# Kernel optimization log

Measured on AMD Instinct MI355X. Metric: run time of the kernel, lower is better.

## Reference

```python
import jax, jax.numpy as jnp
import numpy as np

N_BATCH = 128   # C: number of PWL channels / generator batch
N_PTS = 32768   # N: samples per channel
K_PWL = 20      # breakpoints per piecewise-linear function
LATENT = 8
HID = 8
EPS = 1e-7


def _mlp(z, W1, b1, W2, b2):
    # torch mlp: Linear -> Tanh -> Linear -> Tanh
    h = jnp.tanh(z @ W1 + b1)
    return jnp.tanh(h @ W2 + b2)


def _normalize01(a):
    # per-row min/max normalization, a: [C, N]
    a = a - a.min(axis=1, keepdims=True)
    return a / a.max(axis=1, keepdims=True)


def _calibrate1d(x, xp, yp):
    # x: [N, C], xp/yp: [C, K]
    N, C = x.shape
    K = xp.shape[1]
    bp = jnp.concatenate([x[:, :, None], jnp.broadcast_to(xp[None], (N, C, K))], axis=2)  # [N,C,K+1]
    order = jnp.argsort(bp, axis=2)                       # [N,C,K+1]
    sorted_bp = jnp.take_along_axis(bp, order, axis=2)
    x_idx = jnp.argmin(order, axis=2)                     # rank of x among breakpoints
    cand = x_idx - 1
    start_idx = jnp.where(x_idx == 0, 1, jnp.where(x_idx == K, K - 2, cand))
    end_idx = jnp.where(start_idx == cand, start_idx + 2, start_idx + 1)
    start_x = jnp.take_along_axis(sorted_bp, start_idx[..., None], axis=2)[..., 0]
    end_x = jnp.take_along_axis(sorted_bp, end_idx[..., None], axis=2)[..., 0]
    start_idx2 = jnp.where(x_idx == 0, 0, jnp.where(x_idx == K, K - 2, cand))
    yp_e = jnp.broadcast_to(yp[None], (N, C, K))
    start_y = jnp.take_along_axis(yp_e, start_idx2[..., None], axis=2)[..., 0]
    end_y = jnp.take_along_axis(yp_e, (start_idx2 + 1)[..., None], axis=2)[..., 0]
    return start_y + (x - start_x) * (end_y - start_y) / (end_x - start_x + EPS)


def setup_inputs() -> dict:
    key = jax.random.key(0)
    ks = jax.random.split(key, 16)
    s = 0.5
    f32 = jnp.float32
    return {
        "zf": jax.random.normal(ks[0], (N_BATCH, LATENT), f32),
        "zx": jax.random.normal(ks[1], (N_BATCH, N_PTS, LATENT), f32),
        "ze": jax.random.normal(ks[2], (N_BATCH, N_PTS, LATENT), f32),
        "Wx1": jax.random.normal(ks[3], (LATENT, HID), f32) * s,
        "bx1": jax.random.normal(ks[4], (HID,), f32) * s,
        "Wx2": jax.random.normal(ks[5], (HID, 1), f32) * s,
        "bx2": jax.random.normal(ks[6], (1,), f32) * s,
        "We1": jax.random.normal(ks[7], (LATENT, HID), f32) * s,
        "be1": jax.random.normal(ks[8], (HID,), f32) * s,
        "We2": jax.random.normal(ks[9], (HID, 1), f32) * s,
        "be2": jax.random.normal(ks[10], (1,), f32) * s,
        "Wf1": jax.random.normal(ks[11], (LATENT, HID), f32) * s,
        "bf1": jax.random.normal(ks[12], (HID,), f32) * s,
        "Wf2": jax.random.normal(ks[13], (HID, K_PWL), f32) * s,
        "bf2": jax.random.normal(ks[14], (K_PWL,), f32) * s,
        "directions": jax.random.randint(ks[15], (N_BATCH,), 0, 2) > 0,
    }


def reference(zf, zx, ze, Wx1, bx1, Wx2, bx2, We1, be1, We2, be2, Wf1, bf1, Wf2, bf2, directions):
    # gen_f: random ascending/descending monotone PWL per channel
    pts = _mlp(zf, Wf1, bf1, Wf2, bf2)                        # [C, K]
    asc = jnp.sort(pts, axis=1)
    yp = jnp.where(directions[:, None], asc, asc[:, ::-1])    # [C, K]
    xp = jnp.broadcast_to(jnp.linspace(0.0, 1.0, K_PWL, dtype=pts.dtype)[None, :], yp.shape)
    # forward_x: cause variable, per-channel normalized to [0,1]
    x = _mlp(zx, Wx1, bx1, Wx2, bx2)[..., 0]                  # [C, N]
    x = _normalize01(x).T                                     # [N, C]
    # forward_e: standardized noise (global mean / unbiased std)
    e = _mlp(ze, We1, be1, We2, be2)[..., 0].T                # [N, C]
    e = (e - e.mean()) / e.std(ddof=1)
    # forward_y
    y = _calibrate1d(x, xp, yp) + 0.1 * e                     # [N, C]
    return y
```

## Files before the change

### kernel.cpp

```cpp
#include <hip/hip_runtime.h>

#define C_CH  128
#define NP    32768
#define K_PWL 20
#define LAT   8
#define HID   8
#define SLOTS 32
#define P1PTS 2

__device__ __forceinline__ float fast_tanh(float x) {
    float e = __expf(2.0f * x);
    return fmaf(-2.0f, __builtin_amdgcn_rcpf(e + 1.0f), 1.0f);
}

__device__ __forceinline__ unsigned fenc(float f) {
    unsigned u = __float_as_uint(f);
    return (u & 0x80000000u) ? ~u : (u | 0x80000000u);
}
__device__ __forceinline__ float fdec(unsigned e) {
    unsigned u = (e & 0x80000000u) ? (e ^ 0x80000000u) : ~e;
    return __uint_as_float(u);
}

__device__ __forceinline__ float mlp_eval(const float* W, float4 r0, float4 r1) {
    float acc = W[80];
    #pragma unroll
    for (int j = 0; j < HID; j++) {
        float hh = W[64 + j];
        hh = fmaf(r0.x, W[0 * 8 + j], hh);
        hh = fmaf(r0.y, W[1 * 8 + j], hh);
        hh = fmaf(r0.z, W[2 * 8 + j], hh);
        hh = fmaf(r0.w, W[3 * 8 + j], hh);
        hh = fmaf(r1.x, W[4 * 8 + j], hh);
        hh = fmaf(r1.y, W[5 * 8 + j], hh);
        hh = fmaf(r1.z, W[6 * 8 + j], hh);
        hh = fmaf(r1.w, W[7 * 8 + j], hh);
        acc = fmaf(fast_tanh(hh), W[72 + j], acc);
    }
    return fast_tanh(acc);
}

__global__ void prep(const float* __restrict__ zf,
                     const float* __restrict__ Wf1, const float* __restrict__ bf1,
                     const float* __restrict__ Wf2, const float* __restrict__ bf2,
                     const unsigned char* __restrict__ dirs_raw,
                     float* __restrict__ ypw,
                     unsigned* cminE, unsigned* cmaxE, double* sums) {
    int t = threadIdx.x;
    if (t < C_CH) { cminE[t] = 0xFFFFFFFFu; cmaxE[t] = 0u; }
    if (t < 2 * SLOTS) sums[t] = 0.0;

    __shared__ int is_i32;
    if (t == 0) {
        const int* di = (const int*)dirs_raw;
        int ok = 1;
        for (int i = 0; i < 32; i++) { int v = di[i]; if (v != 0 && v != 1) ok = 0; }
        is_i32 = ok;
    }
    __syncthreads();
    if (t >= C_CH) return;
    int c = t;

    float z[LAT];
    #pragma unroll
    for (int l = 0; l < LAT; l++) z[l] = zf[c * LAT + l];
    float h[HID];
    #pragma unroll
    for (int j = 0; j < HID; j++) {
        float a = bf1[j];
        #pragma unroll
        for (int l = 0; l < LAT; l++) a = fmaf(z[l], Wf1[l * HID + j], a);
        h[j] = fast_tanh(a);
    }
    float p[K_PWL];
    #pragma unroll
    for (int k = 0; k < K_PWL; k++) {
        float a = bf2[k];
        #pragma unroll
        for (int j = 0; j < HID; j++) a = fmaf(h[j], Wf2[j * K_PWL + k], a);
        p[k] = fast_tanh(a);
    }
    for (int i = 1; i < K_PWL; i++) {
        float key = p[i];
        int j = i - 1;
        while (j >= 0 && p[j] > key) { p[j + 1] = p[j]; j--; }
        p[j + 1] = key;
    }
    int dir = is_i32 ? (((const int*)dirs_raw)[c] != 0) : (dirs_raw[c] != 0);
    for (int k = 0; k < K_PWL; k++)
        ypw[c * K_PWL + k] = dir ? p[k] : p[K_PWL - 1 - k];
}

__global__ __launch_bounds__(256, 8)
void pass1t(const float* __restrict__ zx, const float* __restrict__ ze,
            const float* __restrict__ Wx1, const float* __restrict__ bx1,
            const float* __restrict__ Wx2, const float* __restrict__ bx2,
            const float* __restrict__ We1, const float* __restrict__ be1,
            const float* __restrict__ We2, const float* __restrict__ be2,
            float* __restrict__ xtile, float* __restrict__ etile,
            unsigned* __restrict__ cminE, unsigned* __restrict__ cmaxE,
            double* __restrict__ sums) {
    __shared__ float sw[162];
    int t = threadIdx.x;
    if (t < 64)       sw[t] = Wx1[t];
    else if (t < 72)  sw[t] = bx1[t - 64];
    else if (t < 80)  sw[t] = Wx2[t - 72];
    else if (t == 80) sw[80] = bx2[0];
    else if (t < 145) sw[t] = We1[t - 81];
    else if (t < 153) sw[t] = be1[t - 145];
    else if (t < 161) sw[t] = We2[t - 153];
    else if (t == 161) sw[161] = be2[0];
    __syncthreads();

    int c = blockIdx.y;
    int n0 = blockIdx.x * (256 * P1PTS) + t;
    size_t row = (size_t)c * NP;
    const float4* zx4 = (const float4*)(zx + row * LAT);
    const float4* ze4 = (const float4*)(ze + row * LAT);

    float4 ax[P1PTS][2], ae[P1PTS][2];
    #pragma unroll
    for (int k = 0; k < P1PTS; k++) {
        int n = n0 + k * 256;
        ax[k][0] = zx4[2 * n];  ax[k][1] = zx4[2 * n + 1];
        ae[k][0] = ze4[2 * n];  ae[k][1] = ze4[2 * n + 1];
    }

    float xv[P1PTS], ev[P1PTS];
    #pragma unroll
    for (int k = 0; k < P1PTS; k++) xv[k] = mlp_eval(sw, ax[k][0], ax[k][1]);
    #pragma unroll
    for (int k = 0; k < P1PTS; k++) ev[k] = mlp_eval(sw + 81, ae[k][0], ae[k][1]);

    float mn = xv[0], mx = xv[0], s = 0.f, s2 = 0.f;
    int cbase = c * 32;
    #pragma unroll
    for (int k = 0; k < P1PTS; k++) {
        int n = n0 + k * 256;
        int addr = (n >> 5) * (C_CH * 32) + cbase + (n & 31);
        xtile[addr] = xv[k];
        etile[addr] = ev[k];
        mn = fminf(mn, xv[k]); mx = fmaxf(mx, xv[k]);
        s += ev[k]; s2 += ev[k] * ev[k];
    }

    #pragma unroll
    for (int o = 32; o > 0; o >>= 1) {
        mn = fminf(mn, __shfl_down(mn, o));
        mx = fmaxf(mx, __shfl_down(mx, o));
        s += __shfl_down(s, o);
        s2 += __shfl_down(s2, o);
    }
    __shared__ float rmn[4], rmx[4], rs[4], rs2[4];
    int wave = t >> 6, lane = t & 63;
    if (lane == 0) { rmn[wave] = mn; rmx[wave] = mx; rs[wave] = s; rs2[wave] = s2; }
    __syncthreads();
    if (t == 0) {
        for (int w = 1; w < 4; w++) {
            mn = fminf(mn, rmn[w]); mx = fmaxf(mx, rmx[w]);
            s += rs[w]; s2 += rs2[w];
        }
        atomicMin(&cminE[c], fenc(mn));
        atomicMax(&cmaxE[c], fenc(mx));
        int slot = (blockIdx.x + blockIdx.y) & (SLOTS - 1);
        atomicAdd(&sums[2 * slot], (double)s);
        atomicAdd(&sums[2 * slot + 1], (double)s2);
    }
}

__global__ __launch_bounds__(256)
void pass2t(const float* __restrict__ xtile, const float* __restrict__ etile,
            const float* __restrict__ ypw,
            const unsigned* __restrict__ cminE, const unsigned* __restrict__ cmaxE,
            const double* __restrict__ sums,
            float* __restrict__ out) {
    __shared__ float ytile[C_CH * 33];
    __shared__ float syp[C_CH * K_PWL];
    __shared__ float smin[C_CH], sinv[C_CH];
    __shared__ float sstat[2];

    int t = threadIdx.x;
    for (int i = t; i < C_CH * K_PWL; i += 256) syp[i] = ypw[i];
    if (t < C_CH) {
        float mn = fdec(cminE[t]);
        float mx = fdec(cmaxE[t]);
        smin[t] = mn;
        sinv[t] = __builtin_amdgcn_rcpf(mx - mn);
    }
    if (t == 0) {
        double s = 0.0, s2 = 0.0;
        for (int i = 0; i < SLOTS; i++) { s += sums[2 * i]; s2 += sums[2 * i + 1]; }
        double M = (double)C_CH * NP;
        double mean = s / M;
        double var = (s2 - s * s / M) / (M - 1.0);
        sstat[0] = (float)mean;
        sstat[1] = (float)(0.1 / sqrt(var));
    }
    __syncthreads();

    const float INV_DENOM = 1.0f / (1.0f / 19.0f + 1e-7f);
    float mean = sstat[0], escale = sstat[1];
    size_t tbase = (size_t)blockIdx.x * (C_CH * 32);
    int n0 = blockIdx.x * 32;

    #pragma unroll
    for (int i = 0; i < 16; i++) {
        int idx = i * 256 + t;
        int c = idx >> 5;
        int j = idx & 31;
        float x = xtile[tbase + idx];
        float e = etile[tbase + idx];
        float xn = (x - smin[c]) * sinv[c];
        int seg = (int)floorf(xn * 19.0f);
        seg = max(0, min(18, seg));
        float y0 = syp[c * K_PWL + seg];
        float y1 = syp[c * K_PWL + seg + 1];
        float y = fmaf((xn - (float)seg * (1.0f / 19.0f)) * INV_DENOM, y1 - y0, y0);
        y = fmaf(e - mean, escale, y);
        ytile[c * 33 + j] = y;
    }
    __syncthreads();
    #pragma unroll
    for (int i = 0; i < 16; i++) {
        int idx = i * 256 + t;
        int j = idx >> 7;
        int c = idx & 127;
        out[(size_t)(n0 + j) * C_CH + c] = ytile[c * 33 + j];
    }
}

extern "C" void kernel_launch(void* const* d_in, const int* in_sizes, int n_in,
                              void* d_out, int out_size, void* d_ws, size_t ws_size,
                              hipStream_t stream) {
    const float* zf  = (const float*)d_in[0];
    const float* zx  = (const float*)d_in[1];
    const float* ze  = (const float*)d_in[2];
    const float* Wx1 = (const float*)d_in[3];
    const float* bx1 = (const float*)d_in[4];
    const float* Wx2 = (const float*)d_in[5];
    const float* bx2 = (const float*)d_in[6];
    const float* We1 = (const float*)d_in[7];
    const float* be1 = (const float*)d_in[8];
    const float* We2 = (const float*)d_in[9];
    const float* be2 = (const float*)d_in[10];
    const float* Wf1 = (const float*)d_in[11];
    const float* bf1 = (const float*)d_in[12];
    const float* Wf2 = (const float*)d_in[13];
    const float* bf2 = (const float*)d_in[14];
    const unsigned char* dirs = (const unsigned char*)d_in[15];

    float* xtile = (float*)d_ws;
    float* etile = xtile + (size_t)C_CH * NP;
    float* ypw   = etile + (size_t)C_CH * NP;
    unsigned* cminE = (unsigned*)(ypw + C_CH * K_PWL);
    unsigned* cmaxE = cminE + C_CH;
    double* sums = (double*)(cmaxE + C_CH);

    hipLaunchKernelGGL(prep, dim3(1), dim3(256), 0, stream,
                       zf, Wf1, bf1, Wf2, bf2, dirs, ypw, cminE, cmaxE, sums);
    hipLaunchKernelGGL(pass1t, dim3(NP / (256 * P1PTS), C_CH), dim3(256), 0, stream,
                       zx, ze, Wx1, bx1, Wx2, bx2, We1, be1, We2, be2,
                       xtile, etile, cminE, cmaxE, sums);
    hipLaunchKernelGGL(pass2t, dim3(NP / 32), dim3(256), 0, stream,
                       xtile, etile, ypw, cminE, cmaxE, sums, (float*)d_out);
}
```

Baseline: 416.6 us.

## Replace global atomics with per-block partials and fold prep into pass2

Removes the prep kernel launch. pass1 now writes per-block min/max and double sums to partial buffers instead of using global atomics. Every pass2 block recomputes the PWL table with a sorting network and reduces all partials itself. pass1 processes 4 points per thread in a non-unrolled loop with a lower occupancy hint. This trades atomic contention and a launch for redundant reduction and MLP work in each of the 1024 pass2 blocks.

Result: slower. 606.7 us (+45.6%).

```diff
diff --git a/kernel.cpp b/kernel.cpp
--- a/kernel.cpp
+++ b/kernel.cpp
@@ -5,21 +5,12 @@
 #define K_PWL 20
 #define LAT   8
 #define HID   8
-#define SLOTS 32
-#define P1PTS 2
+#define P1PTS 4
+#define QBLK  (NP / (256 * P1PTS))
 
 __device__ __forceinline__ float fast_tanh(float x) {
     float e = __expf(2.0f * x);
     return fmaf(-2.0f, __builtin_amdgcn_rcpf(e + 1.0f), 1.0f);
-}
-
-__device__ __forceinline__ unsigned fenc(float f) {
-    unsigned u = __float_as_uint(f);
-    return (u & 0x80000000u) ? ~u : (u | 0x80000000u);
-}
-__device__ __forceinline__ float fdec(unsigned e) {
-    unsigned u = (e & 0x80000000u) ? (e ^ 0x80000000u) : ~e;
-    return __uint_as_float(u);
 }
 
 __device__ __forceinline__ float mlp_eval(const float* W, float4 r0, float4 r1) {
@@ -40,66 +31,15 @@
     return fast_tanh(acc);
 }
 
-__global__ void prep(const float* __restrict__ zf,
-                     const float* __restrict__ Wf1, const float* __restrict__ bf1,
-                     const float* __restrict__ Wf2, const float* __restrict__ bf2,
-                     const unsigned char* __restrict__ dirs_raw,
-                     float* __restrict__ ypw,
-                     unsigned* cminE, unsigned* cmaxE, double* sums) {
-    int t = threadIdx.x;
-    if (t < C_CH) { cminE[t] = 0xFFFFFFFFu; cmaxE[t] = 0u; }
-    if (t < 2 * SLOTS) sums[t] = 0.0;
-
-    __shared__ int is_i32;
-    if (t == 0) {
-        const int* di = (const int*)dirs_raw;
-        int ok = 1;
-        for (int i = 0; i < 32; i++) { int v = di[i]; if (v != 0 && v != 1) ok = 0; }
-        is_i32 = ok;
-    }
-    __syncthreads();
-    if (t >= C_CH) return;
-    int c = t;
-
-    float z[LAT];
-    #pragma unroll
-    for (int l = 0; l < LAT; l++) z[l] = zf[c * LAT + l];
-    float h[HID];
-    #pragma unroll
-    for (int j = 0; j < HID; j++) {
-        float a = bf1[j];
-        #pragma unroll
-        for (int l = 0; l < LAT; l++) a = fmaf(z[l], Wf1[l * HID + j], a);
-        h[j] = fast_tanh(a);
-    }
-    float p[K_PWL];
-    #pragma unroll
-    for (int k = 0; k < K_PWL; k++) {
-        float a = bf2[k];
-        #pragma unroll
-        for (int j = 0; j < HID; j++) a = fmaf(h[j], Wf2[j * K_PWL + k], a);
-        p[k] = fast_tanh(a);
-    }
-    for (int i = 1; i < K_PWL; i++) {
-        float key = p[i];
-        int j = i - 1;
-        while (j >= 0 && p[j] > key) { p[j + 1] = p[j]; j--; }
-        p[j + 1] = key;
-    }
-    int dir = is_i32 ? (((const int*)dirs_raw)[c] != 0) : (dirs_raw[c] != 0);
-    for (int k = 0; k < K_PWL; k++)
-        ypw[c * K_PWL + k] = dir ? p[k] : p[K_PWL - 1 - k];
-}
-
-__global__ __launch_bounds__(256, 8)
+__global__ __launch_bounds__(256, 4)
 void pass1t(const float* __restrict__ zx, const float* __restrict__ ze,
             const float* __restrict__ Wx1, const float* __restrict__ bx1,
             const float* __restrict__ Wx2, const float* __restrict__ bx2,
             const float* __restrict__ We1, const float* __restrict__ be1,
             const float* __restrict__ We2, const float* __restrict__ be2,
             float* __restrict__ xtile, float* __restrict__ etile,
-            unsigned* __restrict__ cminE, unsigned* __restrict__ cmaxE,
-            double* __restrict__ sums) {
+            float* __restrict__ pminB, float* __restrict__ pmaxB,
+            double* __restrict__ psum) {
     __shared__ float sw[162];
     int t = threadIdx.x;
     if (t < 64)       sw[t] = Wx1[t];
@@ -112,36 +52,27 @@
     else if (t == 161) sw[161] = be2[0];
     __syncthreads();
 
+    int q = blockIdx.x;
     int c = blockIdx.y;
-    int n0 = blockIdx.x * (256 * P1PTS) + t;
+    int n0 = q * (256 * P1PTS) + t;
     size_t row = (size_t)c * NP;
     const float4* zx4 = (const float4*)(zx + row * LAT);
     const float4* ze4 = (const float4*)(ze + row * LAT);
-
-    float4 ax[P1PTS][2], ae[P1PTS][2];
-    #pragma unroll
+    int cbase = c * 32;
+
+    float mn = 3.0e38f, mx = -3.0e38f, s = 0.f, s2 = 0.f;
+    #pragma unroll 1
     for (int k = 0; k < P1PTS; k++) {
         int n = n0 + k * 256;
-        ax[k][0] = zx4[2 * n];  ax[k][1] = zx4[2 * n + 1];
-        ae[k][0] = ze4[2 * n];  ae[k][1] = ze4[2 * n + 1];
-    }
-
-    float xv[P1PTS], ev[P1PTS];
-    #pragma unroll
-    for (int k = 0; k < P1PTS; k++) xv[k] = mlp_eval(sw, ax[k][0], ax[k][1]);
-    #pragma unroll
-    for (int k = 0; k < P1PTS; k++) ev[k] = mlp_eval(sw + 81, ae[k][0], ae[k][1]);
-
-    float mn = xv[0], mx = xv[0], s = 0.f, s2 = 0.f;
-    int cbase = c * 32;
-    #pragma unroll
-    for (int k = 0; k < P1PTS; k++) {
-        int n = n0 + k * 256;
+        float4 a0 = zx4[2 * n], a1 = zx4[2 * n + 1];
+        float4 e0 = ze4[2 * n], e1 = ze4[2 * n + 1];
+        float xv = mlp_eval(sw, a0, a1);
+        float ev = mlp_eval(sw + 81, e0, e1);
         int addr = (n >> 5) * (C_CH * 32) + cbase + (n & 31);
-        xtile[addr] = xv[k];
-        etile[addr] = ev[k];
-        mn = fminf(mn, xv[k]); mx = fmaxf(mx, xv[k]);
-        s += ev[k]; s2 += ev[k] * ev[k];
+        xtile[addr] = xv;
+        etile[addr] = ev;
+        mn = fminf(mn, xv); mx = fmaxf(mx, xv);
+        s += ev; s2 = fmaf(ev, ev, s2);
     }
 
     #pragma unroll
@@ -158,41 +89,106 @@
     if (t == 0) {
         for (int w = 1; w < 4; w++) {
             mn = fminf(mn, rmn[w]); mx = fmaxf(mx, rmx[w]);
-            s += rs[w]; s2 += rs2[w];
-        }
-        atomicMin(&cminE[c], fenc(mn));
-        atomicMax(&cmaxE[c], fenc(mx));
-        int slot = (blockIdx.x + blockIdx.y) & (SLOTS - 1);
-        atomicAdd(&sums[2 * slot], (double)s);
-        atomicAdd(&sums[2 * slot + 1], (double)s2);
+        }
+        int slot = c * QBLK + q;
+        pminB[slot] = mn;
+        pmaxB[slot] = mx;
+        psum[2 * slot]     = (double)rs[0] + (double)rs[1] + (double)rs[2] + (double)rs[3];
+        psum[2 * slot + 1] = (double)rs2[0] + (double)rs2[1] + (double)rs2[2] + (double)rs2[3];
     }
 }
 
 __global__ __launch_bounds__(256)
 void pass2t(const float* __restrict__ xtile, const float* __restrict__ etile,
-            const float* __restrict__ ypw,
-            const unsigned* __restrict__ cminE, const unsigned* __restrict__ cmaxE,
-            const double* __restrict__ sums,
+            const float* __restrict__ zf,
+            const float* __restrict__ Wf1, const float* __restrict__ bf1,
+            const float* __restrict__ Wf2, const float* __restrict__ bf2,
+            const unsigned char* __restrict__ dirs_raw,
+            const float* __restrict__ pminB, const float* __restrict__ pmaxB,
+            const double* __restrict__ psum,
             float* __restrict__ out) {
     __shared__ float ytile[C_CH * 33];
     __shared__ float syp[C_CH * K_PWL];
     __shared__ float smin[C_CH], sinv[C_CH];
+    __shared__ double sred[8];
     __shared__ float sstat[2];
+    __shared__ int is_i32;
 
     int t = threadIdx.x;
-    for (int i = t; i < C_CH * K_PWL; i += 256) syp[i] = ypw[i];
-    if (t < C_CH) {
-        float mn = fdec(cminE[t]);
-        float mx = fdec(cmaxE[t]);
+    int wave = t >> 6, lane = t & 63;
+
+    if (t == 0) {
+        const int* di = (const int*)dirs_raw;
+        int ok = 1;
+        for (int i = 0; i < 32; i++) { int v = di[i]; if (v != 0 && v != 1) ok = 0; }
+        is_i32 = ok;
+    }
+    __syncthreads();
+
+    if (t >= C_CH) {
+        int cc = t - C_CH;
+        float z[LAT];
+        #pragma unroll
+        for (int l = 0; l < LAT; l++) z[l] = zf[cc * LAT + l];
+        float h[HID];
+        #pragma unroll
+        for (int j = 0; j < HID; j++) {
+            float a = bf1[j];
+            #pragma unroll
+            for (int l = 0; l < LAT; l++) a = fmaf(z[l], Wf1[l * HID + j], a);
+            h[j] = fast_tanh(a);
+        }
+        float p[K_PWL];
+        #pragma unroll
+        for (int k = 0; k < K_PWL; k++) {
+            float a = bf2[k];
+            #pragma unroll
+            for (int j = 0; j < HID; j++) a = fmaf(h[j], Wf2[j * K_PWL + k], a);
+            p[k] = fast_tanh(a);
+        }
+        #pragma unroll
+        for (int ph = 0; ph < K_PWL; ph++) {
+            #pragma unroll
+            for (int k = (ph & 1); k + 1 < K_PWL; k += 2) {
+                float lo = fminf(p[k], p[k + 1]);
+                float hi = fmaxf(p[k], p[k + 1]);
+                p[k] = lo; p[k + 1] = hi;
+            }
+        }
+        int dir = is_i32 ? (((const int*)dirs_raw)[cc] != 0) : (dirs_raw[cc] != 0);
+        #pragma unroll
+        for (int k = 0; k < K_PWL; k++)
+            syp[cc * K_PWL + k] = dir ? p[k] : p[K_PWL - 1 - k];
+    } else {
+        float mn = 3.0e38f, mx = -3.0e38f;
+        int base = t * QBLK;
+        #pragma unroll 8
+        for (int qq = 0; qq < QBLK; ++qq) {
+            mn = fminf(mn, pminB[base + qq]);
+            mx = fmaxf(mx, pmaxB[base + qq]);
+        }
         smin[t] = mn;
         sinv[t] = __builtin_amdgcn_rcpf(mx - mn);
     }
+
+    double S = 0.0, S2 = 0.0;
+    for (int i = t; i < C_CH * QBLK; i += 256) {
+        S  += psum[2 * i];
+        S2 += psum[2 * i + 1];
+    }
+    #pragma unroll
+    for (int o = 32; o > 0; o >>= 1) {
+        S  += __shfl_down(S, o);
+        S2 += __shfl_down(S2, o);
+    }
+    if (lane == 0) { sred[wave] = S; sred[4 + wave] = S2; }
+    __syncthreads();
     if (t == 0) {
-        double s = 0.0, s2 = 0.0;
-        for (int i = 0; i < SLOTS; i++) { s += sums[2 * i]; s2 += sums[2 * i + 1]; }
+        S  = sred[0] + sred[1] + sred[2] + sred[3];
+        S2 = sred[4] + sred[5] + sred[6] + sred[7];
         double M = (double)C_CH * NP;
-        double mean = s / M;
-        double var = (s2 - s * s / M) / (M - 1.0);
+        double mean = S / M;
+        double var = (S2 - S * S / M) / (M - 1.0);
         sstat[0] = (float)mean;
         sstat[1] = (float)(0.1 / sqrt(var));
     }
@@ -249,18 +245,16 @@
     const float* bf2 = (const float*)d_in[14];
     const unsigned char* dirs = (const unsigned char*)d_in[15];
 
-    float* xtile = (float*)d_ws;
-    float* etile = xtile + (size_t)C_CH * NP;
-    float* ypw   = etile + (size_t)C_CH * NP;
-    unsigned* cminE = (unsigned*)(ypw + C_CH * K_PWL);
-    unsigned* cmaxE = cminE + C_CH;
-    double* sums = (double*)(cmaxE + C_CH);
-
-    hipLaunchKernelGGL(prep, dim3(1), dim3(256), 0, stream,
-                       zf, Wf1, bf1, Wf2, bf2, dirs, ypw, cminE, cmaxE, sums);
-    hipLaunchKernelGGL(pass1t, dim3(NP / (256 * P1PTS), C_CH), dim3(256), 0, stream,
+    double* psum  = (double*)d_ws;
+    float*  pminB = (float*)(psum + 2 * C_CH * QBLK);
+    float*  pmaxB = pminB + C_CH * QBLK;
+    float*  xtile = pmaxB + C_CH * QBLK;
+    float*  etile = xtile + (size_t)C_CH * NP;
+
+    hipLaunchKernelGGL(pass1t, dim3(QBLK, C_CH), dim3(256), 0, stream,
                        zx, ze, Wx1, bx1, Wx2, bx2, We1, be1, We2, be2,
-                       xtile, etile, cminE, cmaxE, sums);
+                       xtile, etile, pminB, pmaxB, psum);
     hipLaunchKernelGGL(pass2t, dim3(NP / 32), dim3(256), 0, stream,
-                       xtile, etile, ypw, cminE, cmaxE, sums, (float*)d_out);
-}
+                       xtile, etile, zf, Wf1, bf1, Wf2, bf2, dirs,
+                       pminB, pmaxB, psum, (float*)d_out);
+}
```
